# Kernel tuning notes

Hardware: AMD Instinct MI355X
Metric: run time of the kernel (lower is better)

Reference implementation:

```python
import jax, jax.numpy as jnp
import numpy as np
from jax import lax

# problem sizes and solver hyperparameters
B, N, G, T = 8, 128, 100, 24
N_ITERS, LR, RHO = 40, 2e-4, 10.0
VOLL, VOSP = 1000.0, 50.0
RES_UP, RES_DN, RT_UP, RT_DN, RAMP_F = 0.05, 0.02, 2.0, 0.5, 1.0


def setup_inputs() -> dict:
    k = jax.random.split(jax.random.key(0), 8)
    pmin = jax.random.uniform(k[0], (G,), minval=10.0, maxval=50.0)
    pmax = pmin + jax.random.uniform(k[1], (G,), minval=100.0, maxval=300.0)
    b_G = jax.random.uniform(k[2], (G,), minval=10.0, maxval=40.0)
    c_G = jax.random.uniform(k[3], (G,), minval=0.0, maxval=5.0)
    lo, hi = pmin.sum(), pmax.sum()
    forecast = lo + jax.random.uniform(k[4], (B, T)) * 0.5 * (hi - lo)
    omega_scen = 0.05 * hi * jax.random.normal(k[5], (B, N, T))
    om_min = omega_scen.min(axis=1) - 1.0
    om_max = omega_scen.max(axis=1) + 1.0
    eps = jax.random.uniform(k[6], (B,)) * 5.0
    return dict(forecast=forecast, omega_scen=omega_scen, om_min=om_min,
                om_max=om_max, eps=eps, pmin=pmin, pmax=pmax, b_G=b_G, c_G=c_G)


def _solve_one(forecast, omega, om_min, om_max, eps, pmin, pmax, b, c):
    # forecast [T], omega [N,T], om_min/om_max [T], eps scalar
    ramp = pmax * RAMP_F
    rup_p, rdn_p = RES_UP * b, RES_DN * b
    rtu_p, rtd_p = RT_UP * b, RT_DN * b
    dist_max = (om_max[None, :] - omega).sum(-1)   # [N]
    dist_min = (omega - om_min[None, :]).sum(-1)   # [N]

    def objective(v):
        Cost = b[:, None] * v['P'] + c[:, None]
        stage1 = (Cost.sum() + (rup_p[:, None] * v['R_up']).sum()
                  + (rdn_p[:, None] * v['R_dn']).sum())
        Qn = (jnp.einsum('g,ngt->n', rtu_p, v['d_up'])
              + jnp.einsum('g,ngt->n', rtd_p, v['d_dn'])
              + VOLL * v['LS'].sum(-1) + VOSP * v['SP'].sum(-1))
        Qmax = ((rtu_p[:, None] * v['du_max']).sum() + (rtd_p[:, None] * v['dd_max']).sum()
                + VOLL * v['LS_max'].sum() + VOSP * v['SP_max'].sum())
        Qmin = ((rtu_p[:, None] * v['du_min']).sum() + (rtd_p[:, None] * v['dd_min']).sum()
                + VOLL * v['LS_min'].sum() + VOSP * v['SP_min'].sum())
        # epigraph phi[n] >= Qn, >= Qmax - gamma*dist_max, >= Qmin - gamma*dist_min
        phi = jnp.maximum(Qn, jnp.maximum(Qmax - v['gamma'] * dist_max,
                                          Qmin - v['gamma'] * dist_min))
        obj = stage1 + phi.mean() + eps * v['gamma']
        return obj, (phi, Cost)

    def penalty(v):
        relu = jax.nn.relu
        dP = v['P'][:, 1:] - v['P'][:, :-1]
        res = [
            # equality constraints
            v['P'].sum(0) - forecast,
            (v['d_up'] - v['d_dn']).sum(1) + v['LS'] - v['SP'] - omega,
            (v['du_max'] - v['dd_max']).sum(0) + v['LS_max'] - v['SP_max'] - om_max,
            (v['du_min'] - v['dd_min']).sum(0) + v['LS_min'] - v['SP_min'] - om_min,
            # inequality constraints (relu of violation)
            relu(v['P'] + v['R_up'] - pmax[:, None]),
            relu(pmin[:, None] - (v['P'] - v['R_dn'])),
            relu(v['d_up'] - v['R_up'][None]),
            relu(v['d_dn'] - v['R_dn'][None]),
            relu(v['du_max'] - v['R_up']), relu(v['dd_max'] - v['R_dn']),
            relu(v['du_min'] - v['R_up']), relu(v['dd_min'] - v['R_dn']),
            relu(jnp.abs(dP) - ramp[:, None]),
        ]
        total = jnp.zeros(())
        for r in res:
            total = total + (r * r).sum()
        return total

    def loss(v):
        return objective(v)[0] + RHO * penalty(v)

    def project(v):
        v = {kk: jnp.maximum(vv, 0.0) for kk, vv in v.items()}
        v['P'] = jnp.clip(v['P'], pmin[:, None], pmax[:, None])
        return v

    z_gt = jnp.zeros((G, T))
    v0 = {'P': jnp.broadcast_to(0.5 * (pmin + pmax)[:, None], (G, T)),
          'R_up': z_gt, 'R_dn': z_gt,
          'd_up': jnp.zeros((N, G, T)), 'd_dn': jnp.zeros((N, G, T)),
          'LS': jnp.zeros((N, T)), 'SP': jnp.zeros((N, T)),
          'du_max': z_gt, 'dd_max': z_gt,
          'LS_max': jnp.zeros((T,)), 'SP_max': jnp.zeros((T,)),
          'du_min': z_gt, 'dd_min': z_gt,
          'LS_min': jnp.zeros((T,)), 'SP_min': jnp.zeros((T,)),
          'gamma': jnp.zeros(())}
    grad_fn = jax.grad(loss)

    def step(v, _):
        g = grad_fn(v)
        v = jax.tree_util.tree_map(lambda x, gx: x - LR * gx, v, g)
        return project(v), None

    v, _ = lax.scan(step, v0, None, length=N_ITERS)
    obj, (phi, Cost) = objective(v)
    return v['P'], v['R_up'], v['R_dn'], Cost, phi, v['gamma'], obj


def reference(forecast, omega_scen, om_min, om_max, eps, pmin, pmax, b_G, c_G):
    solve = jax.vmap(_solve_one, in_axes=(0, 0, 0, 0, 0, None, None, None, None))
    P, R_up, R_dn, Cost, phi, gamma, obj = solve(
        forecast, omega_scen, om_min, om_max, eps, pmin, pmax, b_G, c_G)
    return P, R_up, R_dn, Cost, phi, gamma, obj
```

## Files before the change

### kernel.cpp

```cpp
#include <hip/hip_runtime.h>
#include <hip/hip_cooperative_groups.h>

namespace cg = cooperative_groups;

#define G_ 100
#define T_ 24
#define NSC 128
#define BATCH 8
#define NITER 40
#define NBLK (BATCH*T_)
#define NTHR 512
#define GMAX 15

typedef unsigned long long u64;

__device__ __forceinline__ u64 gload64(const u64* p){
  return __hip_atomic_load(p, __ATOMIC_RELAXED, __HIP_MEMORY_SCOPE_AGENT);
}
__device__ __forceinline__ void gstore64(u64* p, u64 v){
  __hip_atomic_store(p, v, __ATOMIC_RELAXED, __HIP_MEMORY_SCOPE_AGENT);
}
__device__ __forceinline__ u64 pack(float v, unsigned tag){
  return ((u64)tag<<32) | (u64)__float_as_uint(v);
}
__device__ __forceinline__ float unpackv(u64 x){ return __uint_as_float((unsigned)x); }
__device__ __forceinline__ unsigned unpackt(u64 x){ return (unsigned)(x>>32); }

__device__ __forceinline__ void blockReduce2(float& a, float& b, float* sR){
#pragma unroll
  for (int off=32; off; off>>=1){ a+=__shfl_down(a,off,64); b+=__shfl_down(b,off,64); }
  const int w = threadIdx.x>>6;
  __syncthreads();
  if ((threadIdx.x&63)==0){ sR[w]=a; sR[8+w]=b; }
  __syncthreads();
  a=0.f; b=0.f;
#pragma unroll
  for (int i=0;i<8;++i){ a+=sR[i]; b+=sR[8+i]; }
}

__global__ __launch_bounds__(NTHR, 1) void dro_kernel(
    const float* __restrict__ forecast, const float* __restrict__ omega,
    const float* __restrict__ om_min, const float* __restrict__ om_max,
    const float* __restrict__ eps_in, const float* __restrict__ pmin_g,
    const float* __restrict__ pmax_g, const float* __restrict__ bG,
    const float* __restrict__ cG, float* __restrict__ out, float* __restrict__ ws)
{
  constexpr float LR=2e-4f, VOLL=1000.f, VOSP=50.f, TWO_RHO=20.f, INVN=1.f/128.f;
  const int blk=blockIdx.x;
  const int b=blk&7;
  const int t_own=blk>>3;
  const int tid=threadIdx.x, wave=tid>>6, lane=tid&63;
  int gbase, gcnt;
  if      (wave==0){ gbase=0;  gcnt=14; }
  else if (wave==1){ gbase=0;  gcnt=0;  }
  else if (wave==2){ gbase=14; gcnt=15; }
  else if (wave==3){ gbase=29; gcnt=15; }
  else             { gbase=44+(wave-4)*14; gcnt=14; }
  const bool pA = (wave!=1);

  __shared__ float sRu[2][G_], sRd[2][G_];
  __shared__ float sP[G_];
  __shared__ float sAccU[G_], sAccD[G_];
  __shared__ float sB[G_], sPmin[G_], sPmax[G_], sC[G_];
  __shared__ float sLS[NSC], sSP[NSC], sOm[NSC];
  __shared__ float sGQ[NSC], sR220[NSC];
  __shared__ float sQn[NSC], sDM[NSC], sDm[NSC], sS2[NSC];
  __shared__ float sQp[NSC*9], sSp[NSC*9];
  __shared__ float sQnP[NTHR];
  __shared__ float sRed[40];
  __shared__ float sScal[12];

  u64* W = (u64*)ws;
  u64* QNP = W;
  u64* PP  = W + 73728;
  u64* QS  = W + 147456;
  u64* GAM = W + 156672;
  u64* ST1 = W + 157056;

  const float epsv  = eps_in[b];
  const float omaxT = om_max[b*T_ + t_own];
  const float ominT = om_min[b*T_ + t_own];
  const float fctT  = forecast[b*T_ + t_own];

  float duA[GMAX], duB[GMAX], ddA[GMAX], ddB[GMAX];
  float duMr[2]={0.f,0.f}, ddMr[2]={0.f,0.f}, dumr[2]={0.f,0.f}, ddmr[2]={0.f,0.f};
  float lsm=0.f, spm=0.f, lsn=0.f, spn=0.f;
  float r3reg=0.f, r4reg=0.f, rPreg=0.f;

  if (tid<G_){
    sB[tid]=bG[tid]; sPmin[tid]=pmin_g[tid]; sPmax[tid]=pmax_g[tid]; sC[tid]=cG[tid];
    sRu[0][tid]=0.f; sRd[0][tid]=0.f;
    sAccU[tid]=0.f; sAccD[tid]=0.f;
  }
  if (tid<NSC){
    const int nn=tid;
    sLS[nn]=0.f; sSP[nn]=0.f; sS2[nn]=0.f;
    sOm[nn]=omega[(b*NSC+nn)*T_+t_own];
    float dM=0.f,dm=0.f;
    for (int t=0;t<T_;++t){
      float o=omega[(b*NSC+nn)*T_+t];
      dM+=om_max[b*T_+t]-o; dm+=o-om_min[b*T_+t];
    }
    sDM[nn]=dM; sDm[nn]=dm;
    sQp[nn*9+1]=0.f; sSp[nn*9+1]=0.f;
  }
  __syncthreads();
#pragma unroll
  for (int j=0;j<GMAX;++j){ duA[j]=0.f; duB[j]=0.f; ddA[j]=0.f; ddB[j]=0.f; }
  {
    float p0=0.f;
    if (tid<G_){
      p0=0.5f*(sPmin[tid]+sPmax[tid]);
      sP[tid]=p0;
      gstore64(&PP[b*3072 + t_own*128 + tid], pack(p0,1u));
    }
    if (tid<NSC) gstore64(&QNP[b*3072 + t_own*128 + tid], pack(0.f,1u));
    if (tid<2)   gstore64(&QS[(b*T_ + t_own)*16 + tid], pack(0.f,1u));
    if (t_own==0 && tid==0) gstore64(&GAM[b*16], pack(0.f,1u));
    float rp=p0, dum0=0.f;
    blockReduce2(rp,dum0,sRed);
    r3reg=-omaxT; r4reg=-ominT; rPreg=rp-fctT;
  }
  __syncthreads();

  for (int k=0;k<=NITER;++k){
    const unsigned tg  = (unsigned)(k+1);
    const unsigned tg2 = (unsigned)(k+2);
    const int rb = k%3, wb = (k+1)%3;
    const int kb = k&1, nbuf = kb^1;
    float* sRuC = sRu[kb];  float* sRdC = sRd[kb];
    float* sRuN = sRu[nbuf]; float* sRdN = sRd[nbuf];
    const u64* qnpR = QNP + rb*24576 + b*3072;
    const u64* ppR  = PP  + rb*24576 + b*3072;
    const u64* qsR  = QS  + (rb*BATCH + b)*T_*16;
    const u64* gamR = GAM + (rb*BATCH + b)*16;
    u64* qnpW = QNP + wb*24576 + b*3072 + t_own*128;
    u64* ppW  = PP  + wb*24576 + b*3072 + t_own*128;
    u64* qsW  = QS  + (wb*BATCH + b)*T_*16 + t_own*16;
    u64* gamW = GAM + (wb*BATCH + b)*16;

    const int n = tid&127, sb0 = (tid>>7)*6;
    const bool w0 = (wave==0), w1 = (wave==1), hasG1 = w1 && (lane<36);
    u64 xq[6];
#pragma unroll
    for (int s=0;s<6;++s) xq[s]=gload64(&qnpR[(sb0+s)*128+n]);
    u64 xm0=0,xm1=0,xp0=0,xp1=0,xs0=0,xs1=0,xg=0;
    if (w1){
      if (t_own>0){
        xm0=gload64(&ppR[(t_own-1)*128+lane]);
        if (hasG1) xm1=gload64(&ppR[(t_own-1)*128+lane+64]);
      }
      if (t_own<T_-1){
        xp0=gload64(&ppR[(t_own+1)*128+lane]);
        if (hasG1) xp1=gload64(&ppR[(t_own+1)*128+lane+64]);
      }
    } else if (w0){
      if (lane<T_){ xs0=gload64(&qsR[lane*16]); xs1=gload64(&qsR[lane*16+1]); }
      xg=gload64(gamR);
    }
    for (;;){
      bool pend=false;
#pragma unroll
      for (int s=0;s<6;++s)
        if (unpackt(xq[s])!=tg){ xq[s]=gload64(&qnpR[(sb0+s)*128+n]); pend=true; }
      if (w1){
        if (t_own>0){
          if (unpackt(xm0)!=tg){ xm0=gload64(&ppR[(t_own-1)*128+lane]); pend=true; }
          if (hasG1 && unpackt(xm1)!=tg){ xm1=gload64(&ppR[(t_own-1)*128+lane+64]); pend=true; }
        }
        if (t_own<T_-1){
          if (unpackt(xp0)!=tg){ xp0=gload64(&ppR[(t_own+1)*128+lane]); pend=true; }
          if (hasG1 && unpackt(xp1)!=tg){ xp1=gload64(&ppR[(t_own+1)*128+lane+64]); pend=true; }
        }
      } else if (w0){
        if (lane<T_){
          if (unpackt(xs0)!=tg){ xs0=gload64(&qsR[lane*16]);   pend=true; }
          if (unpackt(xs1)!=tg){ xs1=gload64(&qsR[lane*16+1]); pend=true; }
        }
        if (unpackt(xg)!=tg){ xg=gload64(gamR); pend=true; }
      }
      if (!pend) break;
      __builtin_amdgcn_s_sleep(1);
    }
    sQnP[tid]=unpackv(xq[0])+unpackv(xq[1])+unpackv(xq[2])
             +unpackv(xq[3])+unpackv(xq[4])+unpackv(xq[5]);
    float Qmax=unpackv(xs0), Qmin=unpackv(xs1);
    const float gamma=unpackv(xg);
    __syncthreads();

    if (k==NITER){
      if (w0){
#pragma unroll
        for (int off=32; off; off>>=1){ Qmax+=__shfl_xor(Qmax,off,64); Qmin+=__shfl_xor(Qmin,off,64); }
        if (lane==0){ sScal[2]=Qmax; sScal[3]=Qmin; sScal[4]=gamma; }
      }
      __syncthreads();
      const float Qm=sScal[2], Qn2=sScal[3], gam=sScal[4];
      if (tid<NSC){
        const float qsum=sQnP[tid]+sQnP[tid+128]+sQnP[tid+256]+sQnP[tid+384];
        const float ph=fmaxf(qsum,fmaxf(Qm-gam*sDM[tid],Qn2-gam*sDm[tid]));
        sQn[tid]=ph;
        if (t_own==0) out[76800 + b*NSC + tid]=ph;
      }
      float st=0.f, dum0=0.f;
      if (tid<G_){
        const int g=tid;
        const float Pv=sP[g];
        const float costv=sB[g]*Pv+sC[g];
        st=costv + 0.05f*sB[g]*sRuC[g] + 0.02f*sB[g]*sRdC[g];
        const int o=b*2400 + g*T_ + t_own;
        out[o]=Pv;
        out[19200+o]=sRuC[g];
        out[38400+o]=sRdC[g];
        out[57600+o]=costv;
      }
      blockReduce2(st,dum0,sRed);
      if (tid==0) gstore64(&ST1[(b*T_+t_own)*16], pack(st,99u));
      if (t_own==0){
        if (tid==0) out[77824+b]=gam;
        float s1=0.f;
        if (tid<64){
          u64 xs = (lane<T_)? gload64(&ST1[(b*T_+lane)*16]) : pack(0.f,99u);
          while (unpackt(xs)!=99u){ __builtin_amdgcn_s_sleep(1); xs=gload64(&ST1[(b*T_+lane)*16]); }
          s1=unpackv(xs);
        }
        float pm=(tid<NSC)? sQn[tid] : 0.f;
        blockReduce2(pm,s1,sRed);
        if (tid==0) out[77832+b] = s1 + pm*INVN + epsv*gam;
      }
      break;
    }

    if (w0){
#pragma unroll
      for (int off=32; off; off>>=1){ Qmax+=__shfl_xor(Qmax,off,64); Qmin+=__shfl_xor(Qmin,off,64); }
      float g1l=0.f,g2l=0.f,sgl=0.f;
#pragma unroll
      for (int h=0;h<2;++h){
        const int nn=lane+h*64;
        const float Qn=sQnP[nn]+sQnP[nn+128]+sQnP[nn+256]+sQnP[nn+384];
        const float m1=Qmax-gamma*sDM[nn], m2=Qmin-gamma*sDm[nn];
        const float inner=fmaxf(m1,m2), ph=fmaxf(Qn,inner);
        const float gQn=(Qn==ph?1.f:0.f)/((inner==ph)?2.f:1.f);
        const float gIn=(inner==ph?1.f:0.f)/((Qn==ph)?2.f:1.f);
        const float gm1=gIn*(m1==inner?1.f:0.f)/((m2==inner)?2.f:1.f);
        const float gm2=gIn*(m2==inner?1.f:0.f)/((m1==inner)?2.f:1.f);
        const float gq=gQn*INVN;
        sGQ[nn]=gq;
        g1l+=gm1; g2l+=gm2; sgl+=gm1*sDM[nn]+gm2*sDm[nn];
        const float r2=sS2[nn]+sLS[nn]-sSP[nn]-sOm[nn];
        const float r220=TWO_RHO*r2;
        sR220[nn]=r220;
        sLS[nn]=fmaxf(sLS[nn]-LR*(gq*VOLL+r220),0.f);
        sSP[nn]=fmaxf(sSP[nn]-LR*(gq*VOSP-r220),0.f);
      }
#pragma unroll
      for (int off=32; off; off>>=1){
        g1l+=__shfl_xor(g1l,off,64); g2l+=__shfl_xor(g2l,off,64); sgl+=__shfl_xor(sgl,off,64);
      }
      if (lane==0){ sScal[8]=g1l; sScal[9]=g2l; }
      if (t_own==0 && lane==0)
        gstore64(gamW, pack(fmaxf(gamma-LR*(epsv-INVN*sgl),0.f), tg2));
    }
    __syncthreads();

    if (pA){
      const float gqA=sGQ[lane],    r220A=sR220[lane];
      const float gqB=sGQ[lane+64], r220B=sR220[lane+64];
      float qvA=0.f,qvB=0.f,svA=0.f,svB=0.f;
#pragma unroll
      for (int j=0;j<GMAX;++j){
        if (j<gcnt){
          const int g=gbase+j;
          const float bg=sB[g];
          const float rtu=2.f*bg, rtd=0.5f*bg;
          const float ru=sRuC[g], rd=sRdC[g];
          const float r7A=fmaxf(duA[j]-ru,0.f), r8A=fmaxf(ddA[j]-rd,0.f);
          const float r7B=fmaxf(duB[j]-ru,0.f), r8B=fmaxf(ddB[j]-rd,0.f);
          duA[j]=fmaxf(duA[j]-LR*(gqA*rtu+(r220A+TWO_RHO*r7A)),0.f);
          ddA[j]=fmaxf(ddA[j]-LR*(gqA*rtd+(TWO_RHO*r8A-r220A)),0.f);
          duB[j]=fmaxf(duB[j]-LR*(gqB*rtu+(r220B+TWO_RHO*r7B)),0.f);
          ddB[j]=fmaxf(ddB[j]-LR*(gqB*rtd+(TWO_RHO*r8B-r220B)),0.f);
          qvA+=rtu*duA[j]+rtd*ddA[j];  svA+=duA[j]-ddA[j];
          qvB+=rtu*duB[j]+rtd*ddB[j];  svB+=duB[j]-ddB[j];
        }
      }
      sQp[lane*9+wave]=qvA;      sSp[lane*9+wave]=svA;
      sQp[(lane+64)*9+wave]=qvB; sSp[(lane+64)*9+wave]=svB;
    } else {
      const float r3=__shfl(r3reg,0,64), r4=__shfl(r4reg,0,64), rP=__shfl(rPreg,0,64);
      const float S1s=sScal[8], S2s=sScal[9];
      float pQx=0.f,pQn2=0.f,pr3=0.f,pr4=0.f,pP=0.f;
#pragma unroll
      for (int i=0;i<2;++i){
        if (i==0 || hasG1){
          const int g = lane + i*64;
          const float rupS=sAccU[g], rdnS=sAccD[g];
          const float Pold=sP[g], ru=sRuC[g], rd=sRdC[g];
          const float duMo=duMr[i], ddMo=ddMr[i], dumo=dumr[i], ddmo=ddmr[i];
          const float r5 =fmaxf(Pold+ru-sPmax[g],0.f);
          const float r6 =fmaxf(sPmin[g]-Pold+rd,0.f);
          const float r9 =fmaxf(duMo-ru,0.f), r10=fmaxf(ddMo-rd,0.f);
          const float r11=fmaxf(dumo-ru,0.f), r12=fmaxf(ddmo-rd,0.f);
          const float rampg=sPmax[g];
          float gP=sB[g]+TWO_RHO*(rP+r5-r6);
          if (t_own>0){
            const float dp=Pold-unpackv(i==0?xm0:xm1);
            gP+=TWO_RHO*fmaxf(fabsf(dp)-rampg,0.f)*(dp>=0.f?1.f:-1.f);
          }
          if (t_own<T_-1){
            const float dq=unpackv(i==0?xp0:xp1)-Pold;
            gP-=TWO_RHO*fmaxf(fabsf(dq)-rampg,0.f)*(dq>=0.f?1.f:-1.f);
          }
          const float Pn=fminf(fmaxf(Pold-LR*gP,sPmin[g]),sPmax[g]);
          sP[g]=Pn; gstore64(&ppW[g], pack(Pn,tg2));
          const float rtuB=2.f*sB[g], rtdB=0.5f*sB[g];
          sRuN[g]=fmaxf(ru-LR*(0.05f*sB[g]+TWO_RHO*(r5-rupS-r9-r11)),0.f);
          sRdN[g]=fmaxf(rd-LR*(0.02f*sB[g]+TWO_RHO*(r6-rdnS-r10-r12)),0.f);
          const float duMn=fmaxf(duMo-LR*(INVN*S1s*rtuB+TWO_RHO*( r3+r9 )),0.f);
          const float ddMn=fmaxf(ddMo-LR*(INVN*S1s*rtdB+TWO_RHO*(-r3+r10)),0.f);
          const float dumn=fmaxf(dumo-LR*(INVN*S2s*rtuB+TWO_RHO*( r4+r11)),0.f);
          const float ddmn=fmaxf(ddmo-LR*(INVN*S2s*rtdB+TWO_RHO*(-r4+r12)),0.f);
          duMr[i]=duMn; ddMr[i]=ddMn; dumr[i]=dumn; ddmr[i]=ddmn;
          pQx+=rtuB*duMn+rtdB*ddMn; pQn2+=rtuB*dumn+rtdB*ddmn;
          pr3+=duMn-ddMn; pr4+=dumn-ddmn; pP+=Pn;
        }
      }
#pragma unroll
      for (int off=32; off; off>>=1){
        pQx+=__shfl_down(pQx,off,64);  pQn2+=__shfl_down(pQn2,off,64);
        pr3+=__shfl_down(pr3,off,64);  pr4+=__shfl_down(pr4,off,64);
        pP +=__shfl_down(pP,off,64);
      }
      if (lane==0){
        const float LSMn=fmaxf(lsm-LR*(INVN*S1s*VOLL+TWO_RHO*r3),0.f);
        const float SPMn=fmaxf(spm-LR*(INVN*S1s*VOSP-TWO_RHO*r3),0.f);
        const float LSmn=fmaxf(lsn-LR*(INVN*S2s*VOLL+TWO_RHO*r4),0.f);
        const float SPmn=fmaxf(spn-LR*(INVN*S2s*VOSP-TWO_RHO*r4),0.f);
        lsm=LSMn; spm=SPMn; lsn=LSmn; spn=SPmn;
        gstore64(&qsW[0], pack(pQx + VOLL*LSMn + VOSP*SPMn, tg2));
        gstore64(&qsW[1], pack(pQn2 + VOLL*LSmn + VOSP*SPmn, tg2));
        r3reg=pr3 + LSMn - SPMn - omaxT;
        r4reg=pr4 + LSmn - SPmn - ominT;
        rPreg=pP - fctT;
      }
    }
    __syncthreads();

    if (tid>=256 && tid<384){
      const int nn=tid-256;
      float q=0.f,s=0.f;
#pragma unroll
      for (int w=0;w<8;++w){ q+=sQp[nn*9+w]; s+=sSp[nn*9+w]; }
      sS2[nn]=s;
      q += VOLL*sLS[nn]+VOSP*sSP[nn];
      gstore64(&qnpW[nn], pack(q,tg2));
    }
    if (pA){
#pragma unroll
      for (int j=0;j<GMAX;++j){
        if (j<gcnt){
          const int g=gbase+j;
          const float ru=sRuN[g], rd=sRdN[g];
          float aU=fmaxf(duA[j]-ru,0.f)+fmaxf(duB[j]-ru,0.f);
          float aD=fmaxf(ddA[j]-rd,0.f)+fmaxf(ddB[j]-rd,0.f);
#pragma unroll
          for (int off=32; off; off>>=1){ aU+=__shfl_xor(aU,off,64); aD+=__shfl_xor(aD,off,64); }
          if (lane==0){ sAccU[g]=aU; sAccD[g]=aD; }
        }
      }
    }
  }
}

extern "C" void kernel_launch(void* const* d_in, const int* in_sizes, int n_in,
                              void* d_out, int out_size, void* d_ws, size_t ws_size,
                              hipStream_t stream) {
  const float* forecast = (const float*)d_in[0];
  const float* omega    = (const float*)d_in[1];
  const float* omin     = (const float*)d_in[2];
  const float* omax     = (const float*)d_in[3];
  const float* eps      = (const float*)d_in[4];
  const float* pmin     = (const float*)d_in[5];
  const float* pmax     = (const float*)d_in[6];
  const float* bG       = (const float*)d_in[7];
  const float* cG       = (const float*)d_in[8];
  float* out = (float*)d_out;
  float* ws  = (float*)d_ws;
  void* args[] = { &forecast, &omega, &omin, &omax, &eps, &pmin, &pmax, &bG, &cG, &out, &ws };
  hipLaunchCooperativeKernel((const void*)dro_kernel, dim3(NBLK), dim3(NTHR),
                             args, 0, stream);
}
```

Measured before the change: 449.2 us.

## Restructure per-iteration phases to drop a block barrier and prefetch scalars early

Wave 0's scenario-gradient work (gq, r220) is now computed redundantly in every generator wave, and the gamma, LS/SP and S1/S2 updates move into wave 1. This removes the intermediate __syncthreads and the shared-memory arrays sGQ and sR220. Wave 1 also takes over the Qn packing and publishing, then polls for the next iteration's cross-block Qmax, Qmin and gamma right after its own stores. It keeps them in double-buffered sScal slots, which moves that spin-wait off the critical start of the next iteration. The cost is duplicated ALU work in each wave and longer serial work in wave 1, which may lengthen that wave's critical path.

New measurement: 408.1 us, median of 2. 9.2% less time.

```diff
diff --git a/kernel.cpp b/kernel.cpp
--- a/kernel.cpp
+++ b/kernel.cpp
@@ -63,12 +63,11 @@
   __shared__ float sAccU[G_], sAccD[G_];
   __shared__ float sB[G_], sPmin[G_], sPmax[G_], sC[G_];
   __shared__ float sLS[NSC], sSP[NSC], sOm[NSC];
-  __shared__ float sGQ[NSC], sR220[NSC];
   __shared__ float sQn[NSC], sDM[NSC], sDm[NSC], sS2[NSC];
   __shared__ float sQp[NSC*9], sSp[NSC*9];
   __shared__ float sQnP[NTHR];
   __shared__ float sRed[40];
-  __shared__ float sScal[12];
+  __shared__ float sScal[8];
 
   u64* W = (u64*)ws;
   u64* QNP = W;
@@ -104,6 +103,7 @@
     sDM[nn]=dM; sDm[nn]=dm;
     sQp[nn*9+1]=0.f; sSp[nn*9+1]=0.f;
   }
+  if (tid<6) sScal[tid]=0.f;
   __syncthreads();
 #pragma unroll
   for (int j=0;j<GMAX;++j){ duA[j]=0.f; duB[j]=0.f; ddA[j]=0.f; ddB[j]=0.f; }
@@ -115,8 +115,6 @@
       gstore64(&PP[b*3072 + t_own*128 + tid], pack(p0,1u));
     }
     if (tid<NSC) gstore64(&QNP[b*3072 + t_own*128 + tid], pack(0.f,1u));
-    if (tid<2)   gstore64(&QS[(b*T_ + t_own)*16 + tid], pack(0.f,1u));
-    if (t_own==0 && tid==0) gstore64(&GAM[b*16], pack(0.f,1u));
     float rp=p0, dum0=0.f;
     blockReduce2(rp,dum0,sRed);
     r3reg=-omaxT; r4reg=-ominT; rPreg=rp-fctT;
@@ -128,24 +126,26 @@
     const unsigned tg2 = (unsigned)(k+2);
     const int rb = k%3, wb = (k+1)%3;
     const int kb = k&1, nbuf = kb^1;
+    const int par = k&1, parN = par^1;
     float* sRuC = sRu[kb];  float* sRdC = sRd[kb];
     float* sRuN = sRu[nbuf]; float* sRdN = sRd[nbuf];
     const u64* qnpR = QNP + rb*24576 + b*3072;
     const u64* ppR  = PP  + rb*24576 + b*3072;
-    const u64* qsR  = QS  + (rb*BATCH + b)*T_*16;
-    const u64* gamR = GAM + (rb*BATCH + b)*16;
     u64* qnpW = QNP + wb*24576 + b*3072 + t_own*128;
     u64* ppW  = PP  + wb*24576 + b*3072 + t_own*128;
     u64* qsW  = QS  + (wb*BATCH + b)*T_*16 + t_own*16;
+    const u64* qsN = QS + (wb*BATCH + b)*T_*16;
     u64* gamW = GAM + (wb*BATCH + b)*16;
+    const u64* gamN = gamW;
 
     const int n = tid&127, sb0 = (tid>>7)*6;
-    const bool w0 = (wave==0), w1 = (wave==1), hasG1 = w1 && (lane<36);
+    const bool w1 = (wave==1), hasG1 = w1 && (lane<36);
+    const bool doP = w1 && (k<NITER);
     u64 xq[6];
 #pragma unroll
     for (int s=0;s<6;++s) xq[s]=gload64(&qnpR[(sb0+s)*128+n]);
-    u64 xm0=0,xm1=0,xp0=0,xp1=0,xs0=0,xs1=0,xg=0;
-    if (w1){
+    u64 xm0=0,xm1=0,xp0=0,xp1=0;
+    if (doP){
       if (t_own>0){
         xm0=gload64(&ppR[(t_own-1)*128+lane]);
         if (hasG1) xm1=gload64(&ppR[(t_own-1)*128+lane+64]);
@@ -154,16 +154,13 @@
         xp0=gload64(&ppR[(t_own+1)*128+lane]);
         if (hasG1) xp1=gload64(&ppR[(t_own+1)*128+lane+64]);
       }
-    } else if (w0){
-      if (lane<T_){ xs0=gload64(&qsR[lane*16]); xs1=gload64(&qsR[lane*16+1]); }
-      xg=gload64(gamR);
     }
     for (;;){
       bool pend=false;
 #pragma unroll
       for (int s=0;s<6;++s)
         if (unpackt(xq[s])!=tg){ xq[s]=gload64(&qnpR[(sb0+s)*128+n]); pend=true; }
-      if (w1){
+      if (doP){
         if (t_own>0){
           if (unpackt(xm0)!=tg){ xm0=gload64(&ppR[(t_own-1)*128+lane]); pend=true; }
           if (hasG1 && unpackt(xm1)!=tg){ xm1=gload64(&ppR[(t_own-1)*128+lane+64]); pend=true; }
@@ -172,30 +169,16 @@
           if (unpackt(xp0)!=tg){ xp0=gload64(&ppR[(t_own+1)*128+lane]); pend=true; }
           if (hasG1 && unpackt(xp1)!=tg){ xp1=gload64(&ppR[(t_own+1)*128+lane+64]); pend=true; }
         }
-      } else if (w0){
-        if (lane<T_){
-          if (unpackt(xs0)!=tg){ xs0=gload64(&qsR[lane*16]);   pend=true; }
-          if (unpackt(xs1)!=tg){ xs1=gload64(&qsR[lane*16+1]); pend=true; }
-        }
-        if (unpackt(xg)!=tg){ xg=gload64(gamR); pend=true; }
       }
       if (!pend) break;
       __builtin_amdgcn_s_sleep(1);
     }
     sQnP[tid]=unpackv(xq[0])+unpackv(xq[1])+unpackv(xq[2])
              +unpackv(xq[3])+unpackv(xq[4])+unpackv(xq[5]);
-    float Qmax=unpackv(xs0), Qmin=unpackv(xs1);
-    const float gamma=unpackv(xg);
     __syncthreads();
 
     if (k==NITER){
-      if (w0){
-#pragma unroll
-        for (int off=32; off; off>>=1){ Qmax+=__shfl_xor(Qmax,off,64); Qmin+=__shfl_xor(Qmin,off,64); }
-        if (lane==0){ sScal[2]=Qmax; sScal[3]=Qmin; sScal[4]=gamma; }
-      }
-      __syncthreads();
-      const float Qm=sScal[2], Qn2=sScal[3], gam=sScal[4];
+      const float Qm=sScal[par*3], Qn2=sScal[par*3+1], gam=sScal[par*3+2];
       if (tid<NSC){
         const float qsum=sQnP[tid]+sQnP[tid+128]+sQnP[tid+256]+sQnP[tid+384];
         const float ph=fmaxf(qsum,fmaxf(Qm-gam*sDM[tid],Qn2-gam*sDm[tid]));
@@ -231,42 +214,22 @@
       break;
     }
 
-    if (w0){
-#pragma unroll
-      for (int off=32; off; off>>=1){ Qmax+=__shfl_xor(Qmax,off,64); Qmin+=__shfl_xor(Qmin,off,64); }
-      float g1l=0.f,g2l=0.f,sgl=0.f;
+    const float QmaxS=sScal[par*3], QminS=sScal[par*3+1], gammaS=sScal[par*3+2];
+    float lsR0=0.f, lsR1=0.f, spR0=0.f, spR1=0.f;
+    if (pA){
+      float gqA=0.f,r220A=0.f,gqB=0.f,r220B=0.f;
 #pragma unroll
       for (int h=0;h<2;++h){
         const int nn=lane+h*64;
         const float Qn=sQnP[nn]+sQnP[nn+128]+sQnP[nn+256]+sQnP[nn+384];
-        const float m1=Qmax-gamma*sDM[nn], m2=Qmin-gamma*sDm[nn];
+        const float m1=QmaxS-gammaS*sDM[nn], m2=QminS-gammaS*sDm[nn];
         const float inner=fmaxf(m1,m2), ph=fmaxf(Qn,inner);
         const float gQn=(Qn==ph?1.f:0.f)/((inner==ph)?2.f:1.f);
-        const float gIn=(inner==ph?1.f:0.f)/((Qn==ph)?2.f:1.f);
-        const float gm1=gIn*(m1==inner?1.f:0.f)/((m2==inner)?2.f:1.f);
-        const float gm2=gIn*(m2==inner?1.f:0.f)/((m1==inner)?2.f:1.f);
         const float gq=gQn*INVN;
-        sGQ[nn]=gq;
-        g1l+=gm1; g2l+=gm2; sgl+=gm1*sDM[nn]+gm2*sDm[nn];
         const float r2=sS2[nn]+sLS[nn]-sSP[nn]-sOm[nn];
         const float r220=TWO_RHO*r2;
-        sR220[nn]=r220;
-        sLS[nn]=fmaxf(sLS[nn]-LR*(gq*VOLL+r220),0.f);
-        sSP[nn]=fmaxf(sSP[nn]-LR*(gq*VOSP-r220),0.f);
-      }
-#pragma unroll
-      for (int off=32; off; off>>=1){
-        g1l+=__shfl_xor(g1l,off,64); g2l+=__shfl_xor(g2l,off,64); sgl+=__shfl_xor(sgl,off,64);
-      }
-      if (lane==0){ sScal[8]=g1l; sScal[9]=g2l; }
-      if (t_own==0 && lane==0)
-        gstore64(gamW, pack(fmaxf(gamma-LR*(epsv-INVN*sgl),0.f), tg2));
-    }
-    __syncthreads();
-
-    if (pA){
-      const float gqA=sGQ[lane],    r220A=sR220[lane];
-      const float gqB=sGQ[lane+64], r220B=sR220[lane+64];
+        if (h==0){ gqA=gq; r220A=r220; } else { gqB=gq; r220B=r220; }
+      }
       float qvA=0.f,qvB=0.f,svA=0.f,svB=0.f;
 #pragma unroll
       for (int j=0;j<GMAX;++j){
@@ -288,8 +251,33 @@
       sQp[lane*9+wave]=qvA;      sSp[lane*9+wave]=svA;
       sQp[(lane+64)*9+wave]=qvB; sSp[(lane+64)*9+wave]=svB;
     } else {
+      float g1l=0.f,g2l=0.f,sgl=0.f;
+#pragma unroll
+      for (int h=0;h<2;++h){
+        const int nn=lane+h*64;
+        const float Qn=sQnP[nn]+sQnP[nn+128]+sQnP[nn+256]+sQnP[nn+384];
+        const float m1=QmaxS-gammaS*sDM[nn], m2=QminS-gammaS*sDm[nn];
+        const float inner=fmaxf(m1,m2), ph=fmaxf(Qn,inner);
+        const float gQn=(Qn==ph?1.f:0.f)/((inner==ph)?2.f:1.f);
+        const float gIn=(inner==ph?1.f:0.f)/((Qn==ph)?2.f:1.f);
+        const float gm1=gIn*(m1==inner?1.f:0.f)/((m2==inner)?2.f:1.f);
+        const float gm2=gIn*(m2==inner?1.f:0.f)/((m1==inner)?2.f:1.f);
+        const float gq=gQn*INVN;
+        g1l+=gm1; g2l+=gm2; sgl+=gm1*sDM[nn]+gm2*sDm[nn];
+        const float r2=sS2[nn]+sLS[nn]-sSP[nn]-sOm[nn];
+        const float r220=TWO_RHO*r2;
+        const float lsnew=fmaxf(sLS[nn]-LR*(gq*VOLL+r220),0.f);
+        const float spnew=fmaxf(sSP[nn]-LR*(gq*VOSP-r220),0.f);
+        if (h==0){ lsR0=lsnew; spR0=spnew; } else { lsR1=lsnew; spR1=spnew; }
+      }
+#pragma unroll
+      for (int off=32; off; off>>=1){
+        g1l+=__shfl_xor(g1l,off,64); g2l+=__shfl_xor(g2l,off,64); sgl+=__shfl_xor(sgl,off,64);
+      }
+      const float S1s=g1l, S2s=g2l;
+      if (t_own==0 && lane==0)
+        gstore64(gamW, pack(fmaxf(gammaS-LR*(epsv-INVN*sgl),0.f), tg2));
       const float r3=__shfl(r3reg,0,64), r4=__shfl(r4reg,0,64), rP=__shfl(rPreg,0,64);
-      const float S1s=sScal[8], S2s=sScal[9];
       float pQx=0.f,pQn2=0.f,pr3=0.f,pr4=0.f,pP=0.f;
 #pragma unroll
       for (int i=0;i<2;++i){
@@ -347,15 +335,6 @@
     }
     __syncthreads();
 
-    if (tid>=256 && tid<384){
-      const int nn=tid-256;
-      float q=0.f,s=0.f;
-#pragma unroll
-      for (int w=0;w<8;++w){ q+=sQp[nn*9+w]; s+=sSp[nn*9+w]; }
-      sS2[nn]=s;
-      q += VOLL*sLS[nn]+VOSP*sSP[nn];
-      gstore64(&qnpW[nn], pack(q,tg2));
-    }
     if (pA){
 #pragma unroll
       for (int j=0;j<GMAX;++j){
@@ -369,6 +348,36 @@
           if (lane==0){ sAccU[g]=aU; sAccD[g]=aD; }
         }
       }
+    } else {
+      u64 yq0=0, yq1=0, yg;
+      if (lane<T_){ yq0=gload64(&qsN[lane*16]); yq1=gload64(&qsN[lane*16+1]); }
+      yg=gload64(gamN);
+#pragma unroll
+      for (int h=0;h<2;++h){
+        const int nn=lane+h*64;
+        const float LSn=(h==0?lsR0:lsR1), SPn=(h==0?spR0:spR1);
+        sLS[nn]=LSn; sSP[nn]=SPn;
+        float q=0.f,s=0.f;
+#pragma unroll
+        for (int w=0;w<8;++w){ q+=sQp[nn*9+w]; s+=sSp[nn*9+w]; }
+        sS2[nn]=s;
+        q += VOLL*LSn + VOSP*SPn;
+        gstore64(&qnpW[nn], pack(q,tg2));
+      }
+      for (;;){
+        bool pend=false;
+        if (lane<T_){
+          if (unpackt(yq0)!=tg2){ yq0=gload64(&qsN[lane*16]);   pend=true; }
+          if (unpackt(yq1)!=tg2){ yq1=gload64(&qsN[lane*16+1]); pend=true; }
+        }
+        if (unpackt(yg)!=tg2){ yg=gload64(gamN); pend=true; }
+        if (!pend) break;
+        __builtin_amdgcn_s_sleep(1);
+      }
+      float qmx=(lane<T_)?unpackv(yq0):0.f, qmn=(lane<T_)?unpackv(yq1):0.f;
+#pragma unroll
+      for (int off=32; off; off>>=1){ qmx+=__shfl_xor(qmx,off,64); qmn+=__shfl_xor(qmn,off,64); }
+      if (lane==0){ sScal[parN*3]=qmx; sScal[parN*3+1]=qmn; sScal[parN*3+2]=unpackv(yg); }
     }
   }
 }
```
